# Kernel tuning notes

Measured on AMD Instinct MI355X. Metric: run time of the kernel, lower is better.

Reference implementation:

```python
import jax, jax.numpy as jnp
import numpy as np

EPS = 1e-8  # torch F.cosine_similarity denominator clamp
MARGIN = 0.1  # default M in forward signature


def setup_inputs() -> dict:
    key = jax.random.key(0)
    k1, k2 = jax.random.split(key)
    N, B, D = 4096, 1, 1024
    wsi = jax.random.normal(k1, (N, B, D), dtype=jnp.float32)
    omic = jax.random.normal(k2, (N, B, D), dtype=jnp.float32)
    return {"wsi_embeddings": wsi, "omic_embeddings": omic}


def reference(wsi_embeddings, omic_embeddings):
    # [N, B=1, D] -> [N, D]
    W = wsi_embeddings[:, 0, :]
    O = omic_embeddings[:, 0, :]
    nw = jnp.linalg.norm(W, axis=-1)  # [N]
    no = jnp.linalg.norm(O, axis=-1)  # [N]
    # Full pairwise cosine similarity: S[i, j] = cos(wsi_i, omic_j)
    S = (W @ O.T) / jnp.maximum(nw[:, None] * no[None, :], EPS)  # [N, N]
    d = jnp.diagonal(S)  # cos(wsi_i, omic_i), the "self" similarity
    # off-diagonal hinge: relu(M - cos_ij + cos_ii); diagonal: 1 - cos_ii
    off = jax.nn.relu(MARGIN - S + d[:, None])
    eye = jnp.eye(S.shape[0], dtype=bool)
    L = jnp.where(eye, 1.0 - S, off)
    return jnp.mean(L)
```

## Files before the change

### kernel.cpp

```cpp
#include <hip/hip_runtime.h>
#include <stdint.h>

#define N 4096
#define D 1024
#define MARGIN 0.1f
#define BM 128
#define BN 128
#define BKB 128
#define QS 500.0f
#define INVQS2 (1.0f / (QS * QS))

typedef __attribute__((ext_vector_type(4))) int i32x4;

__global__ __launch_bounds__(256) void prep_kernel(
    const float* __restrict__ W, const float* __restrict__ O,
    uint8_t* __restrict__ Wn, uint8_t* __restrict__ On,
    float* __restrict__ dvec, float* __restrict__ out) {
  const int wv = threadIdx.x >> 6, ln = threadIdx.x & 63;
  const int row = blockIdx.x * 4 + wv;
  if (blockIdx.x == 0 && threadIdx.x == 0) *out = 0.0f;
  const float4* Wr = (const float4*)(W + (size_t)row * D);
  const float4* Or = (const float4*)(O + (size_t)row * D);
  float4 w[4], o[4];
  float sw = 0.f, so = 0.f, sd = 0.f;
  #pragma unroll
  for (int c = 0; c < 4; ++c) {
    w[c] = Wr[ln + c * 64];
    o[c] = Or[ln + c * 64];
    sw += w[c].x * w[c].x + w[c].y * w[c].y + w[c].z * w[c].z + w[c].w * w[c].w;
    so += o[c].x * o[c].x + o[c].y * o[c].y + o[c].z * o[c].z + o[c].w * o[c].w;
    sd += w[c].x * o[c].x + w[c].y * o[c].y + w[c].z * o[c].z + w[c].w * o[c].w;
  }
  #pragma unroll
  for (int off = 1; off < 64; off <<= 1) {
    sw += __shfl_xor(sw, off, 64);
    so += __shfl_xor(so, off, 64);
    sd += __shfl_xor(sd, off, 64);
  }
  const float inw = 1.0f / sqrtf(sw) * QS;
  const float ino = 1.0f / sqrtf(so) * QS;
  if (ln == 0) dvec[row] = sd * inw * ino * INVQS2;
  int* Wo = (int*)(Wn + (size_t)row * D);
  int* Oo = (int*)(On + (size_t)row * D);
  #pragma unroll
  for (int c = 0; c < 4; ++c) {
    int q0 = __float2int_rn(fminf(fmaxf(w[c].x * inw, -127.f), 127.f));
    int q1 = __float2int_rn(fminf(fmaxf(w[c].y * inw, -127.f), 127.f));
    int q2 = __float2int_rn(fminf(fmaxf(w[c].z * inw, -127.f), 127.f));
    int q3 = __float2int_rn(fminf(fmaxf(w[c].w * inw, -127.f), 127.f));
    Wo[ln + c * 64] = (q0 & 255) | ((q1 & 255) << 8) | ((q2 & 255) << 16) |
                      ((q3 & 255) << 24);
    q0 = __float2int_rn(fminf(fmaxf(o[c].x * ino, -127.f), 127.f));
    q1 = __float2int_rn(fminf(fmaxf(o[c].y * ino, -127.f), 127.f));
    q2 = __float2int_rn(fminf(fmaxf(o[c].z * ino, -127.f), 127.f));
    q3 = __float2int_rn(fminf(fmaxf(o[c].w * ino, -127.f), 127.f));
    Oo[ln + c * 64] = (q0 & 255) | ((q1 & 255) << 8) | ((q2 & 255) << 16) |
                      ((q3 & 255) << 24);
  }
}

__global__ __launch_bounds__(256) void gemm_loss_kernel(
    const uint8_t* __restrict__ Wn, const uint8_t* __restrict__ On,
    const float* __restrict__ dvec, float* __restrict__ out) {
  __shared__ __align__(16) uint8_t ldsA0[BM * BKB];
  __shared__ __align__(16) uint8_t ldsB0[BN * BKB];
  __shared__ __align__(16) uint8_t ldsA1[BM * BKB];
  __shared__ __align__(16) uint8_t ldsB1[BN * BKB];
  const int bx = blockIdx.x, by = blockIdx.y;
  const int t = threadIdx.x;
  const int wv = t >> 6, ln = t & 63;
  const int wm = wv >> 1, wn = wv & 1;
  const int lrow = ln & 15;
  const int quad = ln >> 4;
  const int l7 = lrow & 7;

  i32x4 acc[4][4] = {};

  const uint8_t* Ag = Wn + (size_t)(by * BM) * D;
  const uint8_t* Bg = On + (size_t)(bx * BN) * D;

#define STAGE(dstA, dstB, ktv) do {                                          \
    _Pragma("unroll")                                                        \
    for (int c_ = 0; c_ < 4; ++c_) {                                         \
      const int g_ = c_ * 256 + t;        \
      const int r_ = g_ >> 3;             \
      const int gi_ = g_ & 7;                   \
      const int col_ = (gi_ ^ (r_ & 7)) << 4;  \
      __builtin_amdgcn_global_load_lds(                                      \
          (const __attribute__((address_space(1))) void*)(                   \
              Ag + (size_t)r_ * D + (ktv) * BKB + col_),                     \
          (__attribute__((address_space(3))) void*)((dstA) + g_ * 16),       \
          16, 0, 0);                                                         \
      __builtin_amdgcn_global_load_lds(                                      \
          (const __attribute__((address_space(1))) void*)(                   \
              Bg + (size_t)r_ * D + (ktv) * BKB + col_),                     \
          (__attribute__((address_space(3))) void*)((dstB) + g_ * 16),       \
          16, 0, 0);                                                         \
    }                                                                        \
  } while (0)

#define COMPUTE(srcA, srcB) do {                                             \
    _Pragma("unroll")                                                        \
    for (int kk = 0; kk < 2; ++kk) {       \
           \
      const int s0 = ((kk * 4 + quad) ^ l7) << 4;                            \
      i32x4 aF[4], bF[4];                                                    \
      _Pragma("unroll")                                                      \
      for (int mi = 0; mi < 4; ++mi) {                                       \
        const int rr = wm * 64 + mi * 16 + lrow;                             \
        aF[mi] = *(const i32x4*)((srcA) + rr * BKB + s0);                    \
      }                                                                      \
      _Pragma("unroll")                                                      \
      for (int ni = 0; ni < 4; ++ni) {                                       \
        const int cc = wn * 64 + ni * 16 + lrow;                             \
        bF[ni] = *(const i32x4*)((srcB) + cc * BKB + s0);                    \
      }                                                                      \
      _Pragma("unroll")                                                      \
      for (int mi = 0; mi < 4; ++mi)                                         \
        _Pragma("unroll")                                                    \
        for (int ni = 0; ni < 4; ++ni)                                       \
          acc[mi][ni] = __builtin_amdgcn_mfma_i32_16x16x64_i8(               \
              aF[mi], bF[ni], acc[mi][ni], 0, 0, 0);                         \
    }                                                                        \
  } while (0)

  STAGE(ldsA0, ldsB0, 0);
  __syncthreads();
  #pragma unroll
  for (int kp = 0; kp < 4; ++kp) {
    STAGE(ldsA1, ldsB1, kp * 2 + 1);
    COMPUTE(ldsA0, ldsB0);
    __syncthreads();
    if (kp < 3) STAGE(ldsA0, ldsB0, kp * 2 + 2);
    COMPUTE(ldsA1, ldsB1);
    __syncthreads();
  }

  float lsum = 0.0f;
  #pragma unroll
  for (int mi = 0; mi < 4; ++mi) {
    const int gibase = by * BM + wm * 64 + mi * 16 + quad * 4;
    #pragma unroll
    for (int r = 0; r < 4; ++r) {
      const int gi = gibase + r;
      const float di = dvec[gi];
      #pragma unroll
      for (int ni = 0; ni < 4; ++ni) {
        const int gj = bx * BN + wn * 64 + ni * 16 + lrow;
        const float s = (float)acc[mi][ni][r] * INVQS2;
        lsum += (gi == gj) ? (1.0f - s) : fmaxf(MARGIN - s + di, 0.0f);
      }
    }
  }
  #pragma unroll
  for (int off = 32; off; off >>= 1) lsum += __shfl_down(lsum, off, 64);
  __shared__ float bsum[4];
  if (ln == 0) bsum[wv] = lsum;
  __syncthreads();
  if (t == 0) {
    const float tot = (bsum[0] + bsum[1] + bsum[2] + bsum[3]) *
                      (1.0f / ((float)N * (float)N));
    atomicAdd(out, tot);
  }
}

extern "C" void kernel_launch(void* const* d_in, const int* in_sizes, int n_in,
                              void* d_out, int out_size, void* d_ws, size_t ws_size,
                              hipStream_t stream) {
  const float* W = (const float*)d_in[0];
  const float* O = (const float*)d_in[1];
  uint8_t* Wn = (uint8_t*)d_ws;
  uint8_t* On = Wn + (size_t)N * D;
  float* dvec = (float*)(On + (size_t)N * D);
  float* out = (float*)d_out;

  prep_kernel<<<N / 4, 256, 0, stream>>>(W, O, Wn, On, dvec, out);
  dim3 grid(N / BN, N / BM);
  gemm_loss_kernel<<<grid, 256, 0, stream>>>(Wn, On, dvec, out);
}
```

Baseline: 103.0 us.

## Enlarge int8 GEMM tile to 256x256 with 8 waves and explicit vmcnt pipelining

Doubles the block tile to 256x256 with 512 threads, so each wave now computes a 128x64 sub-tile (8x4 MFMA accumulators). This raises on-chip reuse of each staged A/B slice and cuts redundant global/L2 reads. The K loop is fully unrolled with explicit s_waitcnt vmcnt and raw barriers, so the next stage's async global-to-LDS loads can stay in flight while the current stage computes. In exchange, the 128KB of LDS and the higher register use allow about one block per CU. The grid shrinks to 256 blocks, which leaves less latency hiding and makes the load balance depend on the CU count.

```diff
diff --git a/kernel.cpp b/kernel.cpp
--- a/kernel.cpp
+++ b/kernel.cpp
@@ -4,8 +4,8 @@
 #define N 4096
 #define D 1024
 #define MARGIN 0.1f
-#define BM 128
-#define BN 128
+#define BM 256
+#define BN 256
 #define BKB 128
 #define QS 500.0f
 #define INVQS2 (1.0f / (QS * QS))
@@ -59,7 +59,7 @@
   }
 }
 
-__global__ __launch_bounds__(256) void gemm_loss_kernel(
+__global__ __launch_bounds__(512) void gemm_loss_kernel(
     const uint8_t* __restrict__ Wn, const uint8_t* __restrict__ On,
     const float* __restrict__ dvec, float* __restrict__ out) {
   __shared__ __align__(16) uint8_t ldsA0[BM * BKB];
@@ -69,12 +69,12 @@
   const int bx = blockIdx.x, by = blockIdx.y;
   const int t = threadIdx.x;
   const int wv = t >> 6, ln = t & 63;
-  const int wm = wv >> 1, wn = wv & 1;
+  const int wm = wv >> 2, wn = wv & 3;
   const int lrow = ln & 15;
   const int quad = ln >> 4;
   const int l7 = lrow & 7;
 
-  i32x4 acc[4][4] = {};
+  i32x4 acc[8][4] = {};
 
   const uint8_t* Ag = Wn + (size_t)(by * BM) * D;
   const uint8_t* Bg = On + (size_t)(bx * BN) * D;
@@ -82,7 +82,7 @@
 #define STAGE(dstA, dstB, ktv) do {                                          \
     _Pragma("unroll")                                                        \
     for (int c_ = 0; c_ < 4; ++c_) {                                         \
-      const int g_ = c_ * 256 + t;        \
+      const int g_ = c_ * 512 + t;        \
       const int r_ = g_ >> 3;             \
       const int gi_ = g_ & 7;                   \
       const int col_ = (gi_ ^ (r_ & 7)) << 4;  \
@@ -104,10 +104,10 @@
     for (int kk = 0; kk < 2; ++kk) {       \
            \
       const int s0 = ((kk * 4 + quad) ^ l7) << 4;                            \
-      i32x4 aF[4], bF[4];                                                    \
+      i32x4 aF[8], bF[4];                                                    \
       _Pragma("unroll")                                                      \
-      for (int mi = 0; mi < 4; ++mi) {                                       \
-        const int rr = wm * 64 + mi * 16 + lrow;                             \
+      for (int mi = 0; mi < 8; ++mi) {                                       \
+        const int rr = wm * 128 + mi * 16 + lrow;                            \
         aF[mi] = *(const i32x4*)((srcA) + rr * BKB + s0);                    \
       }                                                                      \
       _Pragma("unroll")                                                      \
@@ -116,7 +116,7 @@
         bF[ni] = *(const i32x4*)((srcB) + cc * BKB + s0);                    \
       }                                                                      \
       _Pragma("unroll")                                                      \
-      for (int mi = 0; mi < 4; ++mi)                                         \
+      for (int mi = 0; mi < 8; ++mi)                                         \
         _Pragma("unroll")                                                    \
         for (int ni = 0; ni < 4; ++ni)                                       \
           acc[mi][ni] = __builtin_amdgcn_mfma_i32_16x16x64_i8(               \
@@ -124,22 +124,38 @@
     }                                                                        \
   } while (0)
 
+#define WAITV(n_lit) do {                                                    \
+    asm volatile("s_waitcnt vmcnt(" #n_lit ")" ::: "memory");                \
+    __builtin_amdgcn_sched_barrier(0);                                       \
+  } while (0)
+#define BARRIER() do {                                                       \
+    __builtin_amdgcn_sched_barrier(0);                                       \
+    __builtin_amdgcn_s_barrier();                                            \
+    __builtin_amdgcn_sched_barrier(0);                                       \
+  } while (0)
+
   STAGE(ldsA0, ldsB0, 0);
-  __syncthreads();
-  #pragma unroll
-  for (int kp = 0; kp < 4; ++kp) {
-    STAGE(ldsA1, ldsB1, kp * 2 + 1);
-    COMPUTE(ldsA0, ldsB0);
-    __syncthreads();
-    if (kp < 3) STAGE(ldsA0, ldsB0, kp * 2 + 2);
-    COMPUTE(ldsA1, ldsB1);
-    __syncthreads();
-  }
+  STAGE(ldsA1, ldsB1, 1); WAITV(8); BARRIER();
+  COMPUTE(ldsA0, ldsB0); BARRIER();
+  STAGE(ldsA0, ldsB0, 2); WAITV(8); BARRIER();
+  COMPUTE(ldsA1, ldsB1); BARRIER();
+  STAGE(ldsA1, ldsB1, 3); WAITV(8); BARRIER();
+  COMPUTE(ldsA0, ldsB0); BARRIER();
+  STAGE(ldsA0, ldsB0, 4); WAITV(8); BARRIER();
+  COMPUTE(ldsA1, ldsB1); BARRIER();
+  STAGE(ldsA1, ldsB1, 5); WAITV(8); BARRIER();
+  COMPUTE(ldsA0, ldsB0); BARRIER();
+  STAGE(ldsA0, ldsB0, 6); WAITV(8); BARRIER();
+  COMPUTE(ldsA1, ldsB1); BARRIER();
+  STAGE(ldsA1, ldsB1, 7); WAITV(8); BARRIER();
+  COMPUTE(ldsA0, ldsB0); BARRIER();
+  WAITV(0); BARRIER();
+  COMPUTE(ldsA1, ldsB1);
 
   float lsum = 0.0f;
   #pragma unroll
-  for (int mi = 0; mi < 4; ++mi) {
-    const int gibase = by * BM + wm * 64 + mi * 16 + quad * 4;
+  for (int mi = 0; mi < 8; ++mi) {
+    const int gibase = by * BM + wm * 128 + mi * 16 + quad * 4;
     #pragma unroll
     for (int r = 0; r < 4; ++r) {
       const int gi = gibase + r;
@@ -154,13 +170,14 @@
   }
   #pragma unroll
   for (int off = 32; off; off >>= 1) lsum += __shfl_down(lsum, off, 64);
-  __shared__ float bsum[4];
+  __shared__ float bsum[8];
   if (ln == 0) bsum[wv] = lsum;
   __syncthreads();
   if (t == 0) {
-    const float tot = (bsum[0] + bsum[1] + bsum[2] + bsum[3]) *
-                      (1.0f / ((float)N * (float)N));
-    atomicAdd(out, tot);
+    float tot = 0.f;
+    #pragma unroll
+    for (int i = 0; i < 8; ++i) tot += bsum[i];
+    atomicAdd(out, tot * (1.0f / ((float)N * (float)N)));
   }
 }
 
@@ -176,5 +193,5 @@
 
   prep_kernel<<<N / 4, 256, 0, stream>>>(W, O, Wn, On, dvec, out);
   dim3 grid(N / BN, N / BM);
-  gemm_loss_kernel<<<grid, 256, 0, stream>>>(Wn, On, dvec, out);
+  gemm_loss_kernel<<<grid, 512, 0, stream>>>(Wn, On, dvec, out);
 }
```

Result: faster. 95.26 us (-7.5%).
